# Optimization experiments

Hardware: AMD Instinct MI355X
Metric: run time of the kernel (lower is better)

Reference implementation:

```python
import jax, jax.numpy as jnp
import numpy as np

K1, K2 = 2, 4  # kernels of the two channel groups
BN_EPS = 1e-5


def _neocell_group(x, wa, wb, k):
    # Block-diagonal (a @ x) @ b with a k x k block repeated along the diagonal
    # per channel (NeoCellRepeat): equivalent to blockwise transforms on H and W.
    B, c, H, W = x.shape
    xb = x.reshape(B, c, H // k, k, W // k, k)
    y = jnp.einsum('cpi,bcnimj,cjq->bcnpmq', wa, xb, wb)
    return y.reshape(B, c, H, W)


def setup_inputs() -> dict:
    key = jax.random.key(0)
    ks = jax.random.split(key, 12)
    B, C, H, W = 32, 256, 56, 56
    c1, c2 = 128, 128
    Ci = 4 * C  # inner_mult = 4
    x = jax.random.normal(ks[0], (B, C, H, W), dtype=jnp.float32)
    wa1 = jax.random.normal(ks[1], (c1, K1, K1), dtype=jnp.float32) / np.float32(np.sqrt(K1))
    wb1 = jax.random.normal(ks[2], (c1, K1, K1), dtype=jnp.float32) / np.float32(np.sqrt(K1))
    wa2 = jax.random.normal(ks[3], (c2, K2, K2), dtype=jnp.float32) / np.float32(np.sqrt(K2))
    wb2 = jax.random.normal(ks[4], (c2, K2, K2), dtype=jnp.float32) / np.float32(np.sqrt(K2))
    bn_weight = 1.0 + 0.1 * jax.random.normal(ks[5], (C,), dtype=jnp.float32)
    bn_bias = 0.1 * jax.random.normal(ks[6], (C,), dtype=jnp.float32)
    bn_mean = 0.1 * jax.random.normal(ks[7], (C,), dtype=jnp.float32)
    bn_var = jax.random.uniform(ks[8], (C,), dtype=jnp.float32, minval=0.5, maxval=1.5)
    fc1_w = jax.random.normal(ks[9], (Ci, C), dtype=jnp.float32) / np.float32(np.sqrt(C))
    fc2_w = jax.random.normal(ks[10], (C, Ci), dtype=jnp.float32) / np.float32(np.sqrt(Ci))
    return {"x": x, "wa1": wa1, "wb1": wb1, "wa2": wa2, "wb2": wb2,
            "bn_weight": bn_weight, "bn_bias": bn_bias, "bn_mean": bn_mean,
            "bn_var": bn_var, "fc1_w": fc1_w, "fc2_w": fc2_w}


def reference(x, wa1, wb1, wa2, wb2, bn_weight, bn_bias, bn_mean, bn_var, fc1_w, fc2_w):
    c1 = wa1.shape[0]
    # NeoCell: per-group block-diagonal (a @ x) @ b
    y = jnp.concatenate([
        _neocell_group(x[:, :c1], wa1, wb1, K1),
        _neocell_group(x[:, c1:], wa2, wb2, K2),
    ], axis=1)
    # BatchNorm2d (eval mode, running stats)
    inv = jax.lax.rsqrt(bn_var + BN_EPS)
    scale = (bn_weight * inv)[None, :, None, None]
    shift = (bn_bias - bn_mean * bn_weight * inv)[None, :, None, None]
    y = y * scale + shift
    # chw -> hwc, MLP with exact GELU, hwc -> chw
    y = jnp.transpose(y, (0, 2, 3, 1))
    h = jax.nn.gelu(y @ fc1_w.T, approximate=False)
    y = h @ fc2_w.T
    y = jnp.transpose(y, (0, 3, 1, 2))
    # residual (drop_path = 0)
    return y + x
```

## Files before the change

kernel.cpp:

```cpp
#include <hip/hip_runtime.h>
#include <stdint.h>

typedef __bf16 bf16x8 __attribute__((ext_vector_type(8)));
typedef float f32x4 __attribute__((ext_vector_type(4)));

__device__ __forceinline__ float bf2f(uint16_t u) {
  union { uint32_t i; float f; } v; v.i = ((uint32_t)u) << 16; return v.f;
}
__device__ __forceinline__ uint16_t f2bf(float f) {
  union { float f; uint32_t i; } v; v.f = f;
  uint32_t u = v.i;
  uint32_t r = (u + 0x7FFFu + ((u >> 16) & 1u)) >> 16;
  return (uint16_t)r;
}
__device__ __forceinline__ float fast_gelu(float v) {
  float t2 = v * v;
  float pz = 1.0f + 0.044715f * t2;
  float w = -1.5957691216f * v * pz;
  float e = __expf(w);
  return v * __builtin_amdgcn_rcpf(1.0f + e);
}

__global__ __launch_bounds__(256) void cvt_weights_kernel(
    const float* __restrict__ fc1, const float* __restrict__ fc2,
    uint16_t* __restrict__ fc1b, uint16_t* __restrict__ fc2b)
{
  int i = (blockIdx.x * 256 + threadIdx.x) * 4;
  if (i < 262144) {
    float4 a = *(const float4*)(fc1 + i);
    ushort4 o;
    o.x = f2bf(a.x); o.y = f2bf(a.y); o.z = f2bf(a.z); o.w = f2bf(a.w);
    *(ushort4*)(fc1b + i) = o;
  } else {
    int j = i - 262144;
    float4 a = *(const float4*)(fc2 + j);
    ushort4 o;
    o.x = f2bf(a.x); o.y = f2bf(a.y); o.z = f2bf(a.z); o.w = f2bf(a.w);
    *(ushort4*)(fc2b + j) = o;
  }
}

__global__ __launch_bounds__(128) void neocell_bn_kernel(
    const float* __restrict__ x,
    const float* __restrict__ wa1, const float* __restrict__ wb1,
    const float* __restrict__ wa2, const float* __restrict__ wb2,
    const float* __restrict__ bnw, const float* __restrict__ bnb,
    const float* __restrict__ bnm, const float* __restrict__ bnv,
    uint16_t* __restrict__ y1)
{
  __shared__ uint16_t lx[128 * 226];
  const int t = threadIdx.x;
  const int strip = blockIdx.x;
  const int b = blockIdx.y;
  const int half = blockIdx.z;
  const int h0 = strip * 4;

  for (int i = 0; i < 56; ++i) {
    int l = t + i * 128;
    int c = l / 56;
    int r = l - c * 56;
    const float* g = x + (size_t)(b * 256 + half * 128 + c) * 3136
                       + h0 * 56 + r * 4;
    float4 v = *(const float4*)g;
    ushort4 o;
    o.x = f2bf(v.x); o.y = f2bf(v.y); o.z = f2bf(v.z); o.w = f2bf(v.w);
    *(ushort4*)(lx + c * 226 + r * 4) = o;
  }
  __syncthreads();

  const int a = t & 63;
  const int p = t >> 6;
  const int c0 = half * 128 + 2 * a;

  float sc[2], sh[2];
#pragma unroll
  for (int ch = 0; ch < 2; ++ch) {
    int cg = c0 + ch;
    sc[ch] = bnw[cg] * rsqrtf(bnv[cg] + 1e-5f);
    sh[ch] = bnb[cg] - bnm[cg] * sc[ch];
  }
  const size_t pgbase = (size_t)b * 3136 + (size_t)h0 * 56;

  if (half == 0) {
    float A[2][2][2], Bm[2][2][2];
#pragma unroll
    for (int ch = 0; ch < 2; ++ch)
#pragma unroll
      for (int i = 0; i < 2; ++i)
#pragma unroll
        for (int j = 0; j < 2; ++j) {
          A[ch][i][j]  = wa1[(2 * a + ch) * 4 + i * 2 + j];
          Bm[ch][i][j] = wb1[(2 * a + ch) * 4 + i * 2 + j];
        }
    for (int m = 0; m < 28; ++m) {
      float O[2][2][2];
#pragma unroll
      for (int ch = 0; ch < 2; ++ch) {
        const uint16_t* lc = lx + (2 * a + ch) * 226 + (2 * p) * 56 + m * 2;
        uint32_t w0 = *(const uint32_t*)lc;
        uint32_t w1 = *(const uint32_t*)(lc + 56);
        float X[2][2];
        X[0][0] = bf2f((uint16_t)w0); X[0][1] = bf2f((uint16_t)(w0 >> 16));
        X[1][0] = bf2f((uint16_t)w1); X[1][1] = bf2f((uint16_t)(w1 >> 16));
        float T[2][2];
#pragma unroll
        for (int pp = 0; pp < 2; ++pp)
#pragma unroll
          for (int j = 0; j < 2; ++j)
            T[pp][j] = A[ch][pp][0] * X[0][j] + A[ch][pp][1] * X[1][j];
#pragma unroll
        for (int pp = 0; pp < 2; ++pp)
#pragma unroll
          for (int q = 0; q < 2; ++q)
            O[ch][pp][q] = (T[pp][0] * Bm[ch][0][q] + T[pp][1] * Bm[ch][1][q])
                           * sc[ch] + sh[ch];
      }
#pragma unroll
      for (int pp = 0; pp < 2; ++pp)
#pragma unroll
        for (int q = 0; q < 2; ++q) {
          uint32_t pk = (uint32_t)f2bf(O[0][pp][q])
                      | ((uint32_t)f2bf(O[1][pp][q]) << 16);
          size_t pg = pgbase + (size_t)(2 * p + pp) * 56 + (m * 2 + q);
          *(uint32_t*)(y1 + pg * 256 + c0) = pk;
        }
    }
  } else {
    float A[2][4][4], Bm[2][4][4];
#pragma unroll
    for (int ch = 0; ch < 2; ++ch)
#pragma unroll
      for (int i = 0; i < 4; ++i)
#pragma unroll
        for (int j = 0; j < 4; ++j) {
          A[ch][i][j]  = wa2[(2 * a + ch) * 16 + i * 4 + j];
          Bm[ch][i][j] = wb2[(2 * a + ch) * 16 + i * 4 + j];
        }
    for (int mm = 0; mm < 7; ++mm) {
      int m = 2 * mm + p;
      float O[2][4][4];
#pragma unroll
      for (int ch = 0; ch < 2; ++ch) {
        float X[4][4];
#pragma unroll
        for (int i = 0; i < 4; ++i) {
          const uint16_t* lc = lx + (2 * a + ch) * 226 + i * 56 + m * 4;
          uint32_t w0 = *(const uint32_t*)lc;
          uint32_t w1 = *(const uint32_t*)(lc + 2);
          X[i][0] = bf2f((uint16_t)w0); X[i][1] = bf2f((uint16_t)(w0 >> 16));
          X[i][2] = bf2f((uint16_t)w1); X[i][3] = bf2f((uint16_t)(w1 >> 16));
        }
        float T[4][4];
#pragma unroll
        for (int pp = 0; pp < 4; ++pp)
#pragma unroll
          for (int j = 0; j < 4; ++j)
            T[pp][j] = A[ch][pp][0] * X[0][j] + A[ch][pp][1] * X[1][j]
                     + A[ch][pp][2] * X[2][j] + A[ch][pp][3] * X[3][j];
#pragma unroll
        for (int pp = 0; pp < 4; ++pp)
#pragma unroll
          for (int q = 0; q < 4; ++q)
            O[ch][pp][q] = (T[pp][0] * Bm[ch][0][q] + T[pp][1] * Bm[ch][1][q]
                          + T[pp][2] * Bm[ch][2][q] + T[pp][3] * Bm[ch][3][q])
                           * sc[ch] + sh[ch];
      }
#pragma unroll
      for (int pp = 0; pp < 4; ++pp)
#pragma unroll
        for (int q = 0; q < 4; ++q) {
          uint32_t pk = (uint32_t)f2bf(O[0][pp][q])
                      | ((uint32_t)f2bf(O[1][pp][q]) << 16);
          size_t pg = pgbase + (size_t)pp * 56 + (m * 4 + q);
          *(uint32_t*)(y1 + pg * 256 + c0) = pk;
        }
    }
  }
}

template <int KD, int EPI>
__global__ __launch_bounds__(256) void gemm_bt_kernel(
    const uint16_t* __restrict__ A,
    const uint16_t* __restrict__ Bw,
    uint16_t* __restrict__ Cb16,
    float* __restrict__ Cf32,
    const float* __restrict__ Xres,
    int chunk_pix0)
{
  __shared__ uint16_t lds[16640];
  uint16_t* ldsA = lds;
  uint16_t* ldsB = lds + 4096;

  const int tid = threadIdx.x;
  const int lane = tid & 63;
  const int wid = tid >> 6;
  const int wm = wid & 1;
  const int wn = wid >> 1;
  const int fm = lane & 15;
  const int fq = lane >> 4;

  const size_t arow0 = (size_t)blockIdx.y * 128;
  const size_t brow0 = (size_t)blockIdx.x * 128;

  f32x4 acc[4][4];
#pragma unroll
  for (int i = 0; i < 4; ++i)
#pragma unroll
    for (int j = 0; j < 4; ++j) { f32x4 z = {0.f, 0.f, 0.f, 0.f}; acc[i][j] = z; }

  const int q0 = tid, q1 = tid + 256;
  const int r0 = q0 >> 2, kk0 = q0 & 3;
  const int r1 = q1 >> 2, kk1 = q1 & 3;
  const uint16_t* a0 = A + (arow0 + r0) * KD + kk0 * 8;
  const uint16_t* a1 = A + (arow0 + r1) * KD + kk1 * 8;
  const uint16_t* b0 = Bw + (brow0 + r0) * KD + kk0 * 8;
  const uint16_t* b1 = Bw + (brow0 + r1) * KD + kk1 * 8;

  for (int k0 = 0; k0 < KD; k0 += 32) {
    __syncthreads();
    __builtin_amdgcn_global_load_lds(
        (const __attribute__((address_space(1))) void*)(a0 + k0),
        (__attribute__((address_space(3))) void*)(ldsA + q0 * 8), 16, 0, 0);
    __builtin_amdgcn_global_load_lds(
        (const __attribute__((address_space(1))) void*)(a1 + k0),
        (__attribute__((address_space(3))) void*)(ldsA + q1 * 8), 16, 0, 0);
    __builtin_amdgcn_global_load_lds(
        (const __attribute__((address_space(1))) void*)(b0 + k0),
        (__attribute__((address_space(3))) void*)(ldsB + q0 * 8), 16, 0, 0);
    __builtin_amdgcn_global_load_lds(
        (const __attribute__((address_space(1))) void*)(b1 + k0),
        (__attribute__((address_space(3))) void*)(ldsB + q1 * 8), 16, 0, 0);
    __syncthreads();

    bf16x8 af[4], bfr[4];
#pragma unroll
    for (int mt = 0; mt < 4; ++mt)
      af[mt] = *(const bf16x8*)(const void*)
               (ldsA + (wm * 64 + mt * 16 + fm) * 32 + fq * 8);
#pragma unroll
    for (int nt = 0; nt < 4; ++nt)
      bfr[nt] = *(const bf16x8*)(const void*)
                (ldsB + (wn * 64 + nt * 16 + fm) * 32 + fq * 8);
#pragma unroll
    for (int mt = 0; mt < 4; ++mt)
#pragma unroll
      for (int nt = 0; nt < 4; ++nt)
        acc[mt][nt] = __builtin_amdgcn_mfma_f32_16x16x32_bf16(
            af[mt], bfr[nt], acc[mt][nt], 0, 0, 0);
  }

  if (EPI == 0) {
#pragma unroll
    for (int mt = 0; mt < 4; ++mt) {
      const size_t rb = arow0 + wm * 64 + mt * 16 + fq * 4;
#pragma unroll
      for (int nt = 0; nt < 4; ++nt) {
        const size_t n = brow0 + wn * 64 + nt * 16 + fm;
#pragma unroll
        for (int r = 0; r < 4; ++r)
          Cb16[(rb + r) * 1024 + n] = f2bf(fast_gelu(acc[mt][nt][r]));
      }
    }
  } else {
    __syncthreads();
#pragma unroll
    for (int mt = 0; mt < 4; ++mt) {
      int mbase = wm * 64 + mt * 16 + fq * 4;
#pragma unroll
      for (int nt = 0; nt < 4; ++nt) {
        int n = wn * 64 + nt * 16 + fm;
#pragma unroll
        for (int r = 0; r < 4; ++r)
          lds[n * 130 + mbase + r] = f2bf(acc[mt][nt][r]);
      }
    }
    __syncthreads();
    const int pl0 = tid & 31;
    const int cw = tid >> 5;
#pragma unroll
    for (int it = 0; it < 16; ++it) {
      int ch = cw + it * 8;
      int cgl = (int)brow0 + ch;
#pragma unroll
      for (int e = 0; e < 4; ++e) {
        int pl = pl0 + e * 32;
        uint32_t pg = (uint32_t)chunk_pix0 + blockIdx.y * 128u + (uint32_t)pl;
        uint32_t bimg = pg / 3136u;
        uint32_t rem = pg - bimg * 3136u;
        size_t addr = ((size_t)bimg * 256 + cgl) * 3136 + rem;
        Cf32[addr] = bf2f(lds[ch * 130 + pl]) + Xres[addr];
      }
    }
  }
}

extern "C" void kernel_launch(void* const* d_in, const int* in_sizes, int n_in,
                              void* d_out, int out_size, void* d_ws,
                              size_t ws_size, hipStream_t stream)
{
  const float* x   = (const float*)d_in[0];
  const float* wa1 = (const float*)d_in[1];
  const float* wb1 = (const float*)d_in[2];
  const float* wa2 = (const float*)d_in[3];
  const float* wb2 = (const float*)d_in[4];
  const float* bnw = (const float*)d_in[5];
  const float* bnb = (const float*)d_in[6];
  const float* bnm = (const float*)d_in[7];
  const float* bnv = (const float*)d_in[8];
  const float* fc1 = (const float*)d_in[9];
  const float* fc2 = (const float*)d_in[10];
  float* out = (float*)d_out;

  uint16_t* fc1b = (uint16_t*)d_ws;
  uint16_t* fc2b = fc1b + 262144;
  uint16_t* y1 = fc2b + 262144;
  const size_t y1_elems = (size_t)100352 * 256;
  uint16_t* h = y1 + y1_elems;

  const long tiles_total = 784;
  const size_t fixed_bytes = (size_t)262144 * 4 + y1_elems * 2;
  long tiles_chunk = 1;
  if (ws_size > fixed_bytes + 262144) {
    tiles_chunk = (long)((ws_size - fixed_bytes) / (128ul * 1024ul * 2ul));
    if (tiles_chunk > tiles_total) tiles_chunk = tiles_total;
    if (tiles_chunk < 1) tiles_chunk = 1;
  }

  cvt_weights_kernel<<<512, 256, 0, stream>>>(fc1, fc2, fc1b, fc2b);
  neocell_bn_kernel<<<dim3(14, 32, 2), 128, 0, stream>>>(
      x, wa1, wb1, wa2, wb2, bnw, bnb, bnm, bnv, y1);

  for (long t0 = 0; t0 < tiles_total; t0 += tiles_chunk) {
    long T = tiles_total - t0;
    if (T > tiles_chunk) T = tiles_chunk;
    gemm_bt_kernel<256, 0><<<dim3(8, (uint32_t)T), 256, 0, stream>>>(
        y1 + (size_t)t0 * 128 * 256, fc1b, h, nullptr, nullptr, 0);
    gemm_bt_kernel<1024, 1><<<dim3(2, (uint32_t)T), 256, 0, stream>>>(
        h, fc2b, nullptr, out, x, (int)(t0 * 128));
  }
}
```

Baseline: 443.2 us.

## Fuse fc1+GELU and fc2 GEMMs into one MLP kernel keeping hidden in LDS

Replaces the two separate GEMM launches, which round-trip the hidden activation through global memory, with a single kernel. Each block handles 128 pixels and loops over 8 hidden chunks of 128. For each chunk it computes the fc1 GEMM, applies GELU, writes the result into a swizzled LDS buffer, then accumulates the fc2 product into registers covering all 256 output channels. This removes the 100352x1024 bf16 hidden write and read. The cost is a large register footprint (128 accumulator vectors plus 64), fewer blocks (784 CTAs), no B-tile reuse across blocks for the weight loads, and possible register spills or low occupancy.

```diff
diff --git a/kernel.cpp b/kernel.cpp
--- a/kernel.cpp
+++ b/kernel.cpp
@@ -19,6 +19,11 @@
   float w = -1.5957691216f * v * pz;
   float e = __expf(w);
   return v * __builtin_amdgcn_rcpf(1.0f + e);
+}
+__device__ __forceinline__ void gld16(uint16_t* l, const uint16_t* g) {
+  __builtin_amdgcn_global_load_lds(
+      (const __attribute__((address_space(1))) void*)g,
+      (__attribute__((address_space(3))) void*)l, 16, 0, 0);
 }
 
 __global__ __launch_bounds__(256) void cvt_weights_kernel(
@@ -178,18 +183,15 @@
   }
 }
 
-template <int KD, int EPI>
-__global__ __launch_bounds__(256) void gemm_bt_kernel(
-    const uint16_t* __restrict__ A,
-    const uint16_t* __restrict__ Bw,
-    uint16_t* __restrict__ Cb16,
-    float* __restrict__ Cf32,
-    const float* __restrict__ Xres,
-    int chunk_pix0)
+__global__ __launch_bounds__(256, 2) void fused_mlp_kernel(
+    const uint16_t* __restrict__ y1, const uint16_t* __restrict__ fc1b,
+    const uint16_t* __restrict__ fc2b, float* __restrict__ out,
+    const float* __restrict__ Xres)
 {
-  __shared__ uint16_t lds[16640];
+  __shared__ uint16_t lds[24576];
   uint16_t* ldsA = lds;
   uint16_t* ldsB = lds + 4096;
+  uint16_t* ldsH = lds + 8192;
 
   const int tid = threadIdx.x;
   const int lane = tid & 63;
@@ -199,79 +201,118 @@
   const int fm = lane & 15;
   const int fq = lane >> 4;
 
-  const size_t arow0 = (size_t)blockIdx.y * 128;
-  const size_t brow0 = (size_t)blockIdx.x * 128;
-
-  f32x4 acc[4][4];
-#pragma unroll
-  for (int i = 0; i < 4; ++i)
-#pragma unroll
-    for (int j = 0; j < 4; ++j) { f32x4 z = {0.f, 0.f, 0.f, 0.f}; acc[i][j] = z; }
+  const size_t pix0 = (size_t)blockIdx.x * 128;
 
   const int q0 = tid, q1 = tid + 256;
-  const int r0 = q0 >> 2, kk0 = q0 & 3;
-  const int r1 = q1 >> 2, kk1 = q1 & 3;
-  const uint16_t* a0 = A + (arow0 + r0) * KD + kk0 * 8;
-  const uint16_t* a1 = A + (arow0 + r1) * KD + kk1 * 8;
-  const uint16_t* b0 = Bw + (brow0 + r0) * KD + kk0 * 8;
-  const uint16_t* b1 = Bw + (brow0 + r1) * KD + kk1 * 8;
-
-  for (int k0 = 0; k0 < KD; k0 += 32) {
+  const int r0 = q0 >> 2, s0 = q0 & 3;
+  const int r1 = q1 >> 2, s1 = q1 & 3;
+  const uint16_t* ya = y1 + (pix0 + r0) * 256 + s0 * 8;
+  const uint16_t* yb = y1 + (pix0 + r1) * 256 + s1 * 8;
+
+  f32x4 oacc[8][4];
+#pragma unroll
+  for (int i = 0; i < 8; ++i)
+#pragma unroll
+    for (int j = 0; j < 4; ++j) { f32x4 z = {0.f, 0.f, 0.f, 0.f}; oacc[i][j] = z; }
+
+  for (int kc = 0; kc < 8; ++kc) {
+    const uint16_t* w1b = fc1b + (size_t)(kc * 128) * 256;
+    f32x4 c1[4][4];
+#pragma unroll
+    for (int i = 0; i < 4; ++i)
+#pragma unroll
+      for (int j = 0; j < 4; ++j) { f32x4 z = {0.f, 0.f, 0.f, 0.f}; c1[i][j] = z; }
+
+    for (int j0 = 0; j0 < 256; j0 += 32) {
+      __syncthreads();
+      gld16(ldsA + q0 * 8, w1b + r0 * 256 + s0 * 8 + j0);
+      gld16(ldsA + q1 * 8, w1b + r1 * 256 + s1 * 8 + j0);
+      gld16(ldsB + q0 * 8, ya + j0);
+      gld16(ldsB + q1 * 8, yb + j0);
+      __syncthreads();
+
+      bf16x8 af[4], bfr[4];
+#pragma unroll
+      for (int mt = 0; mt < 4; ++mt)
+        af[mt] = *(const bf16x8*)(const void*)
+                 (ldsA + (wm * 64 + mt * 16 + fm) * 32 + fq * 8);
+#pragma unroll
+      for (int nt = 0; nt < 4; ++nt)
+        bfr[nt] = *(const bf16x8*)(const void*)
+                  (ldsB + (wn * 64 + nt * 16 + fm) * 32 + fq * 8);
+#pragma unroll
+      for (int mt = 0; mt < 4; ++mt)
+#pragma unroll
+        for (int nt = 0; nt < 4; ++nt)
+          c1[mt][nt] = __builtin_amdgcn_mfma_f32_16x16x32_bf16(
+              af[mt], bfr[nt], c1[mt][nt], 0, 0, 0);
+    }
+
+    {
+      const int p_base = wn * 64 + fm;
+      const int kkb_base = wm * 64 + fq * 4;
+#pragma unroll
+      for (int nt = 0; nt < 4; ++nt) {
+        const int p = p_base + nt * 16;
+        const int sw = (p & 7) << 4;
+        char* rowp = (char*)ldsH + p * 256;
+#pragma unroll
+        for (int mt = 0; mt < 4; ++mt) {
+          const int kkb = kkb_base + mt * 16;
+          uint32_t lo = (uint32_t)f2bf(fast_gelu(c1[mt][nt][0]))
+                      | ((uint32_t)f2bf(fast_gelu(c1[mt][nt][1])) << 16);
+          uint32_t hi = (uint32_t)f2bf(fast_gelu(c1[mt][nt][2]))
+                      | ((uint32_t)f2bf(fast_gelu(c1[mt][nt][3])) << 16);
+          *(uint64_t*)(rowp + ((kkb * 2) ^ sw)) = ((uint64_t)hi << 32) | lo;
+        }
+      }
+    }
+
+    const uint16_t* w2b = fc2b + kc * 128;
+    for (int k2 = 0; k2 < 128; k2 += 32) {
+      __syncthreads();
+#pragma unroll
+      for (int s = 0; s < 4; ++s) {
+        int q = tid + s * 256;
+        int c = q >> 2, sg = q & 3;
+        gld16(lds + q * 8, w2b + c * 1024 + k2 + sg * 8);
+      }
+      __syncthreads();
+
+      bf16x8 ah[8], bw[4];
+#pragma unroll
+      for (int mt = 0; mt < 8; ++mt) {
+        int p = mt * 16 + fm;
+        ah[mt] = *(const bf16x8*)(const void*)
+                 ((char*)ldsH + p * 256 + (((k2 + fq * 8) * 2) ^ ((p & 7) << 4)));
+      }
+#pragma unroll
+      for (int nt = 0; nt < 4; ++nt)
+        bw[nt] = *(const bf16x8*)(const void*)
+                 (lds + (wid * 64 + nt * 16 + fm) * 32 + fq * 8);
+#pragma unroll
+      for (int mt = 0; mt < 8; ++mt)
+#pragma unroll
+        for (int nt = 0; nt < 4; ++nt)
+          oacc[mt][nt] = __builtin_amdgcn_mfma_f32_16x16x32_bf16(
+              ah[mt], bw[nt], oacc[mt][nt], 0, 0, 0);
+    }
+  }
+
+#pragma unroll
+  for (int hh = 0; hh < 2; ++hh) {
     __syncthreads();
-    __builtin_amdgcn_global_load_lds(
-        (const __attribute__((address_space(1))) void*)(a0 + k0),
-        (__attribute__((address_space(3))) void*)(ldsA + q0 * 8), 16, 0, 0);
-    __builtin_amdgcn_global_load_lds(
-        (const __attribute__((address_space(1))) void*)(a1 + k0),
-        (__attribute__((address_space(3))) void*)(ldsA + q1 * 8), 16, 0, 0);
-    __builtin_amdgcn_global_load_lds(
-        (const __attribute__((address_space(1))) void*)(b0 + k0),
-        (__attribute__((address_space(3))) void*)(ldsB + q0 * 8), 16, 0, 0);
-    __builtin_amdgcn_global_load_lds(
-        (const __attribute__((address_space(1))) void*)(b1 + k0),
-        (__attribute__((address_space(3))) void*)(ldsB + q1 * 8), 16, 0, 0);
-    __syncthreads();
-
-    bf16x8 af[4], bfr[4];
-#pragma unroll
-    for (int mt = 0; mt < 4; ++mt)
-      af[mt] = *(const bf16x8*)(const void*)
-               (ldsA + (wm * 64 + mt * 16 + fm) * 32 + fq * 8);
-#pragma unroll
-    for (int nt = 0; nt < 4; ++nt)
-      bfr[nt] = *(const bf16x8*)(const void*)
-                (ldsB + (wn * 64 + nt * 16 + fm) * 32 + fq * 8);
-#pragma unroll
-    for (int mt = 0; mt < 4; ++mt)
-#pragma unroll
-      for (int nt = 0; nt < 4; ++nt)
-        acc[mt][nt] = __builtin_amdgcn_mfma_f32_16x16x32_bf16(
-            af[mt], bfr[nt], acc[mt][nt], 0, 0, 0);
-  }
-
-  if (EPI == 0) {
-#pragma unroll
-    for (int mt = 0; mt < 4; ++mt) {
-      const size_t rb = arow0 + wm * 64 + mt * 16 + fq * 4;
-#pragma unroll
-      for (int nt = 0; nt < 4; ++nt) {
-        const size_t n = brow0 + wn * 64 + nt * 16 + fm;
-#pragma unroll
-        for (int r = 0; r < 4; ++r)
-          Cb16[(rb + r) * 1024 + n] = f2bf(fast_gelu(acc[mt][nt][r]));
-      }
-    }
-  } else {
-    __syncthreads();
-#pragma unroll
-    for (int mt = 0; mt < 4; ++mt) {
-      int mbase = wm * 64 + mt * 16 + fq * 4;
-#pragma unroll
-      for (int nt = 0; nt < 4; ++nt) {
-        int n = wn * 64 + nt * 16 + fm;
-#pragma unroll
-        for (int r = 0; r < 4; ++r)
-          lds[n * 130 + mbase + r] = f2bf(acc[mt][nt][r]);
+    if ((wid >> 1) == hh) {
+#pragma unroll
+      for (int mt = 0; mt < 8; ++mt) {
+        int m = mt * 16 + fq * 4;
+#pragma unroll
+        for (int nt = 0; nt < 4; ++nt) {
+          int nl = (wid & 1) * 64 + nt * 16 + fm;
+#pragma unroll
+          for (int r = 0; r < 4; ++r)
+            lds[nl * 130 + m + r] = f2bf(oacc[mt][nt][r]);
+        }
       }
     }
     __syncthreads();
@@ -280,15 +321,15 @@
 #pragma unroll
     for (int it = 0; it < 16; ++it) {
       int ch = cw + it * 8;
-      int cgl = (int)brow0 + ch;
+      int cgl = hh * 128 + ch;
 #pragma unroll
       for (int e = 0; e < 4; ++e) {
         int pl = pl0 + e * 32;
-        uint32_t pg = (uint32_t)chunk_pix0 + blockIdx.y * 128u + (uint32_t)pl;
+        uint32_t pg = (uint32_t)pix0 + (uint32_t)pl;
         uint32_t bimg = pg / 3136u;
         uint32_t rem = pg - bimg * 3136u;
         size_t addr = ((size_t)bimg * 256 + cgl) * 3136 + rem;
-        Cf32[addr] = bf2f(lds[ch * 130 + pl]) + Xres[addr];
+        out[addr] = bf2f(lds[ch * 130 + pl]) + Xres[addr];
       }
     }
   }
@@ -314,28 +355,9 @@
   uint16_t* fc1b = (uint16_t*)d_ws;
   uint16_t* fc2b = fc1b + 262144;
   uint16_t* y1 = fc2b + 262144;
-  const size_t y1_elems = (size_t)100352 * 256;
-  uint16_t* h = y1 + y1_elems;
-
-  const long tiles_total = 784;
-  const size_t fixed_bytes = (size_t)262144 * 4 + y1_elems * 2;
-  long tiles_chunk = 1;
-  if (ws_size > fixed_bytes + 262144) {
-    tiles_chunk = (long)((ws_size - fixed_bytes) / (128ul * 1024ul * 2ul));
-    if (tiles_chunk > tiles_total) tiles_chunk = tiles_total;
-    if (tiles_chunk < 1) tiles_chunk = 1;
-  }
 
   cvt_weights_kernel<<<512, 256, 0, stream>>>(fc1, fc2, fc1b, fc2b);
   neocell_bn_kernel<<<dim3(14, 32, 2), 128, 0, stream>>>(
       x, wa1, wb1, wa2, wb2, bnw, bnb, bnm, bnv, y1);
-
-  for (long t0 = 0; t0 < tiles_total; t0 += tiles_chunk) {
-    long T = tiles_total - t0;
-    if (T > tiles_chunk) T = tiles_chunk;
-    gemm_bt_kernel<256, 0><<<dim3(8, (uint32_t)T), 256, 0, stream>>>(
-        y1 + (size_t)t0 * 128 * 256, fc1b, h, nullptr, nullptr, 0);
-    gemm_bt_kernel<1024, 1><<<dim3(2, (uint32_t)T), 256, 0, stream>>>(
-        h, fc2b, nullptr, out, x, (int)(t0 * 128));
-  }
-}
+  fused_mlp_kernel<<<784, 256, 0, stream>>>(y1, fc1b, fc2b, out, x);
+}
```

Result: slower. 546.3 us (+23.3%).
